# Optimization experiments

Hardware: AMD Instinct MI355X
Metric: run time of the kernel (lower is better)

## Reference

```python
import jax, jax.numpy as jnp
import numpy as np

K = 20
EPS = 1e-5
SLOPE = 0.2

def _knn_idx(x, k):
    # x: [B, C, N] -> idx [B, N, k] of nearest neighbors (includes self)
    xx = jnp.sum(x * x, axis=1)                      # [B, N]
    inner = jnp.einsum('bcn,bcm->bnm', x, x)          # [B, N, N]
    dist = xx[:, :, None] - 2.0 * inner + xx[:, None, :]
    _, idx = jax.lax.top_k(-dist, k)                  # [B, N, k]
    return idx

def _get_attention_feature(x, k):
    # x: [B, C, N] -> [B, N, k, 2C] = cat([x_j - x_i, x_i])
    idx = _knn_idx(x, k)
    xt = jnp.transpose(x, (0, 2, 1))                  # [B, N, C]
    nbr = jax.vmap(lambda pts, ids: pts[ids])(xt, idx)  # [B, N, k, C]
    ctr = xt[:, :, None, :]                           # [B, N, 1, C]
    return jnp.concatenate([nbr - ctr, jnp.broadcast_to(ctr, nbr.shape)], axis=-1)

def _gat(feat, W, a):
    # feat: [B, N, k, 2C]; W: [2C, out_c]; a: [4, H] with H = out_c // 4
    B, N, k, _ = feat.shape
    out_c = W.shape[1]
    H = out_c // 4
    hw = jnp.einsum('bnkf,fd->bnkd', feat, W).reshape(B, N, k, H, 4)
    t = jax.nn.leaky_relu(hw, SLOPE)
    logits = jnp.einsum('bnkhd,dh->bnkh', t, a)
    w = jax.nn.softmax(logits, axis=2)                # softmax over neighbors k
    out = jnp.einsum('bnkh,bnkhd->bnhd', w, hw).reshape(B, N, out_c)
    out = jax.nn.leaky_relu(out, SLOPE)
    return jnp.transpose(out, (0, 2, 1))              # [B, out_c, N]

def _bn(x, gamma, beta):
    # BatchNorm1d in training mode (batch stats) over [B, C, N]
    mu = jnp.mean(x, axis=(0, 2), keepdims=True)
    var = jnp.var(x, axis=(0, 2), keepdims=True)
    xn = (x - mu) / jnp.sqrt(var + EPS)
    return xn * gamma[None, :, None] + beta[None, :, None]

def _layer(x, W, a, gamma, beta):
    feat = _get_attention_feature(x, K)
    h = _gat(feat, W, a)
    h = _bn(h, gamma, beta)
    return jax.nn.leaky_relu(h, SLOPE)

def setup_inputs() -> dict:
    key = jax.random.key(0)
    ks = jax.random.split(key, 10)
    dims = [(3, 64), (64, 64), (64, 128)]
    inp = {'x': jax.random.normal(ks[0], (8, 3, 2048), dtype=jnp.float32)}
    for i, (cin, cout) in enumerate(dims):
        inp[f'W{i}'] = jax.random.normal(ks[1 + 3 * i], (2 * cin, cout), dtype=jnp.float32) * 0.1
        inp[f'a{i}'] = jax.random.normal(ks[2 + 3 * i], (4, cout // 4), dtype=jnp.float32) * 0.1
        inp[f'g{i}'] = jnp.ones((cout,), dtype=jnp.float32)
        inp[f'b{i}'] = jnp.zeros((cout,), dtype=jnp.float32)
    return inp

def reference(x, W0, a0, g0, b0, W1, a1, g1, b1, W2, a2, g2, b2):
    x = _layer(x, W0, a0, g0, b0)
    x = _layer(x, W1, a1, g1, b1)
    x = _layer(x, W2, a2, g2, b2)
    return x  # [B, 128, N]
```

## Files before the change

kernel.cpp:

```cpp
#include <hip/hip_runtime.h>
#include <float.h>
#include <math.h>

#define BATCH 8
#define NPTS  2048
#define KNN   20
#define BN    (BATCH*NPTS)
#define SLOPE 0.2f
#define BNEPS 1e-5f

__global__ void xx_kernel(const float* __restrict__ x, float* __restrict__ xx, int C) {
    int p = blockIdx.x * 256 + threadIdx.x;
    int b = p >> 11, n = p & (NPTS - 1);
    const float* xb = x + (size_t)b * C * NPTS;
    float s = 0.f;
    for (int c = 0; c < C; ++c) { float v = xb[(size_t)c * NPTS + n]; s = fmaf(v, v, s); }
    xx[p] = s;
}

__device__ __forceinline__ void gload_lds16(const float* g, float* l) {
    __builtin_amdgcn_global_load_lds(
        (const __attribute__((address_space(1))) void*)g,
        (__attribute__((address_space(3))) void*)l, 16, 0, 0);
}

template<int C>
__global__ __launch_bounds__(256, 2) void knn8_kernel(const float* __restrict__ x,
                                                      const float* __restrict__ xx,
                                                      float* __restrict__ pv,
                                                      int* __restrict__ pi) {
    constexpr int ROWS = 32, CHUNK = 128, HALF = 1024, NCH = HALF / CHUNK;
    constexpr int CP     = (C > 32) ? 32 : C;
    constexpr int PASSES = C / CP;
    constexpr int NST    = (CP * 32 + 255) / 256;

    __shared__ __align__(16) float xrT[C][32];
    __shared__ __align__(16) union ULX {
        struct { float xc[CP][CHUNK]; float dt[ROWS][129]; float thrG[8][32]; } s;
        struct { float v[8][KNN][ROWS]; unsigned short i[8][KNN][ROWS]; } L;
    } u;

    int t    = threadIdx.x;
    int b    = blockIdx.x >> 7;
    int tile = (blockIdx.x >> 1) & 63;
    int half = blockIdx.x & 1;
    int r0   = tile * ROWS;
    int j0h  = half * HALF;
    const float* xb  = x  + (size_t)b * C * NPTS;
    const float* xxb = xx + (size_t)b * NPTS;

    int ty = t >> 5, tx = t & 31;
    int ty4 = ty * 4, tx4 = tx * 4;

    for (int f = t; f < ROWS * C; f += 256) {
        int r = f & 31, c = f >> 5;
        xrT[c][r] = xb[(size_t)c * NPTS + r0 + r];
    }
    u.s.thrG[ty][tx] = FLT_MAX;
#pragma unroll
    for (int k = 0; k < NST; ++k) {
        int i = t + 256 * k;
        if (i < CP * 32) {
            int c = i >> 5, j = (i & 31) * 4;
            gload_lds16(xb + (size_t)c * NPTS + j0h + j, &u.s.xc[0][0] + (size_t)i * 4);
        }
    }

    float lv[KNN]; int li[KNN];
#pragma unroll
    for (int s = 0; s < KNN; ++s) { lv[s] = FLT_MAX; li[s] = 0x7fffffff; }

    __syncthreads();

    for (int ch = 0; ch < NCH; ++ch) {
        int j0g = j0h + ch * CHUNK;

        float4 a0 = {0,0,0,0}, a1 = {0,0,0,0}, a2 = {0,0,0,0}, a3 = {0,0,0,0};

#pragma unroll 4
        for (int c = 0; c < CP; ++c) {
            float4 rv = *(const float4*)&xrT[c][ty4];
            float4 cv = *(const float4*)&u.s.xc[c][tx4];
            a0.x = fmaf(rv.x, cv.x, a0.x); a0.y = fmaf(rv.x, cv.y, a0.y);
            a0.z = fmaf(rv.x, cv.z, a0.z); a0.w = fmaf(rv.x, cv.w, a0.w);
            a1.x = fmaf(rv.y, cv.x, a1.x); a1.y = fmaf(rv.y, cv.y, a1.y);
            a1.z = fmaf(rv.y, cv.z, a1.z); a1.w = fmaf(rv.y, cv.w, a1.w);
            a2.x = fmaf(rv.z, cv.x, a2.x); a2.y = fmaf(rv.z, cv.y, a2.y);
            a2.z = fmaf(rv.z, cv.z, a2.z); a2.w = fmaf(rv.z, cv.w, a2.w);
            a3.x = fmaf(rv.w, cv.x, a3.x); a3.y = fmaf(rv.w, cv.y, a3.y);
            a3.z = fmaf(rv.w, cv.z, a3.z); a3.w = fmaf(rv.w, cv.w, a3.w);
        }

        if constexpr (PASSES == 2) {
            __syncthreads();
#pragma unroll
            for (int k = 0; k < NST; ++k) {
                int i = t + 256 * k;
                int c = i >> 5, j = (i & 31) * 4;
                gload_lds16(xb + (size_t)(CP + c) * NPTS + j0g + j,
                            &u.s.xc[0][0] + (size_t)i * 4);
            }
            __syncthreads();
#pragma unroll 4
            for (int c = 0; c < CP; ++c) {
                float4 rv = *(const float4*)&xrT[CP + c][ty4];
                float4 cv = *(const float4*)&u.s.xc[c][tx4];
                a0.x = fmaf(rv.x, cv.x, a0.x); a0.y = fmaf(rv.x, cv.y, a0.y);
                a0.z = fmaf(rv.x, cv.z, a0.z); a0.w = fmaf(rv.x, cv.w, a0.w);
                a1.x = fmaf(rv.y, cv.x, a1.x); a1.y = fmaf(rv.y, cv.y, a1.y);
                a1.z = fmaf(rv.y, cv.z, a1.z); a1.w = fmaf(rv.y, cv.w, a1.w);
                a2.x = fmaf(rv.z, cv.x, a2.x); a2.y = fmaf(rv.z, cv.y, a2.y);
                a2.z = fmaf(rv.z, cv.z, a2.z); a2.w = fmaf(rv.z, cv.w, a2.w);
                a3.x = fmaf(rv.w, cv.x, a3.x); a3.y = fmaf(rv.w, cv.y, a3.y);
                a3.z = fmaf(rv.w, cv.z, a3.z); a3.w = fmaf(rv.w, cv.w, a3.w);
            }
        }

        {
            float4 xq = *(const float4*)&xxb[j0g + tx4];
            u.s.dt[ty4 + 0][tx4 + 0] = xq.x - 2.f * a0.x;
            u.s.dt[ty4 + 0][tx4 + 1] = xq.y - 2.f * a0.y;
            u.s.dt[ty4 + 0][tx4 + 2] = xq.z - 2.f * a0.z;
            u.s.dt[ty4 + 0][tx4 + 3] = xq.w - 2.f * a0.w;
            u.s.dt[ty4 + 1][tx4 + 0] = xq.x - 2.f * a1.x;
            u.s.dt[ty4 + 1][tx4 + 1] = xq.y - 2.f * a1.y;
            u.s.dt[ty4 + 1][tx4 + 2] = xq.z - 2.f * a1.z;
            u.s.dt[ty4 + 1][tx4 + 3] = xq.w - 2.f * a1.w;
            u.s.dt[ty4 + 2][tx4 + 0] = xq.x - 2.f * a2.x;
            u.s.dt[ty4 + 2][tx4 + 1] = xq.y - 2.f * a2.y;
            u.s.dt[ty4 + 2][tx4 + 2] = xq.z - 2.f * a2.z;
            u.s.dt[ty4 + 2][tx4 + 3] = xq.w - 2.f * a2.w;
            u.s.dt[ty4 + 3][tx4 + 0] = xq.x - 2.f * a3.x;
            u.s.dt[ty4 + 3][tx4 + 1] = xq.y - 2.f * a3.y;
            u.s.dt[ty4 + 3][tx4 + 2] = xq.z - 2.f * a3.z;
            u.s.dt[ty4 + 3][tx4 + 3] = xq.w - 2.f * a3.w;
        }
        __syncthreads();

        if (ch + 1 < NCH) {
            int j0n = j0g + CHUNK;
#pragma unroll
            for (int k = 0; k < NST; ++k) {
                int i = t + 256 * k;
                if (i < CP * 32) {
                    int c = i >> 5, j = (i & 31) * 4;
                    gload_lds16(xb + (size_t)c * NPTS + j0n + j,
                                &u.s.xc[0][0] + (size_t)i * 4);
                }
            }
        }

        {
            int r = tx;
            float thr = u.s.thrG[0][r];
#pragma unroll
            for (int g = 1; g < 8; ++g) thr = fminf(thr, u.s.thrG[g][r]);

            const float* drow = &u.s.dt[r][ty * 16];
#pragma unroll
            for (int m = 0; m < 16; ++m) {
                float v = drow[m];
                if (v < lv[KNN - 1] && v <= thr) {
                    lv[KNN - 1] = v; li[KNN - 1] = j0g + ty * 16 + m;
#pragma unroll
                    for (int s = KNN - 1; s > 0; --s) {
                        if (lv[s] < lv[s - 1]) {
                            float tv = lv[s]; lv[s] = lv[s - 1]; lv[s - 1] = tv;
                            int   ti = li[s]; li[s] = li[s - 1]; li[s - 1] = ti;
                        }
                    }
                }
            }
        }
        u.s.thrG[ty][tx] = lv[KNN - 1];
        __syncthreads();
    }

    {
        int r = tx, g = ty;
#pragma unroll
        for (int s = 0; s < KNN; ++s) {
            u.L.v[g][s][r] = lv[s];
            u.L.i[g][s][r] = (unsigned short)(li[s] & 0xFFFF);
        }
    }
    __syncthreads();

    if (t < ROWS) {
        int r = t;
        float hv[8]; int hi[8]; int pp[8];
#pragma unroll
        for (int g = 0; g < 8; ++g) { pp[g] = 0; hv[g] = u.L.v[g][0][r]; hi[g] = u.L.i[g][0][r]; }
        size_t base = ((size_t)(b * NPTS + r0 + r) * 2 + half) * KNN;
        for (int o = 0; o < KNN; ++o) {
            float bv = hv[0]; int bi = hi[0]; int bg = 0;
#pragma unroll
            for (int g = 1; g < 8; ++g)
                if (hv[g] < bv || (hv[g] == bv && hi[g] < bi)) { bv = hv[g]; bi = hi[g]; bg = g; }
            pv[base + o] = bv; pi[base + o] = bi;
#pragma unroll
            for (int g = 0; g < 8; ++g)
                if (bg == g) {
                    ++pp[g];
                    bool ok = pp[g] < KNN;
                    int q = ok ? pp[g] : KNN - 1;
                    float nv = u.L.v[g][q][r]; int ni = u.L.i[g][q][r];
                    hv[g] = ok ? nv : FLT_MAX;
                    hi[g] = ok ? ni : 0x7fffffff;
                }
        }
    }
}

__global__ void knnmerge_kernel(const float* __restrict__ pv, const int* __restrict__ pi,
                                int* __restrict__ idx) {
    int p = blockIdx.x * 256 + threadIdx.x;
    size_t b0 = (size_t)p * 2 * KNN, b1 = b0 + KNN;
    int ia = 0, ib = 0;
    int* op = idx + (size_t)p * KNN;
    for (int o = 0; o < KNN; ++o) {
        float va = pv[b0 + ia], vb = pv[b1 + ib];
        int   ja = pi[b0 + ia], jb = pi[b1 + ib];
        bool takeA = (va < vb) || (va == vb && ja < jb);
        op[o] = takeA ? ja : jb;
        ia += takeA ? 1 : 0;
        ib += takeA ? 0 : 1;
    }
}

__global__ void proj_kernel(const float* __restrict__ x, const float* __restrict__ W,
                            float* __restrict__ y, float* __restrict__ z, int C, int Cout) {
    int p = blockIdx.x;
    int b = p >> 11, n = p & (NPTS - 1);
    int j = threadIdx.x;
    __shared__ float xc[64];
    if (j < C) xc[j] = x[(size_t)b * C * NPTS + (size_t)j * NPTS + n];
    __syncthreads();
    float sy = 0.f, sz = 0.f;
    for (int c = 0; c < C; ++c) {
        float xv = xc[c];
        float wt = W[c * Cout + j];
        float wb = W[(C + c) * Cout + j];
        sy = fmaf(xv, wt, sy);
        sz = fmaf(xv, wb - wt, sz);
    }
    y[(size_t)p * Cout + j] = sy;
    z[(size_t)p * Cout + j] = sz;
}

template<int CO>
__global__ __launch_bounds__(256) void attn_kernel(const float* __restrict__ y,
                                                   const float* __restrict__ z,
                                                   const int* __restrict__ idx,
                                                   const float* __restrict__ a,
                                                   float* __restrict__ hout) {
    constexpr int NCH = CO / 64;
    constexpr int H   = CO / 4;
    int wv = threadIdx.x >> 6;
    int l  = threadIdx.x & 63;
    int p  = blockIdx.x * 4 + wv;
    int b  = p >> 11;
    float hw[NCH][KNN], lg[NCH][KNN], zv[NCH], av[NCH];
#pragma unroll
    for (int q = 0; q < NCH; ++q) {
        int c = l + 64 * q;
        zv[q] = z[(size_t)p * CO + c];
        av[q] = a[(c & 3) * H + (c >> 2)];
    }
    const int* ip = idx + (size_t)p * KNN;
#pragma unroll
    for (int j = 0; j < KNN; ++j) {
        int m = ip[j];
        const float* yr = y + ((size_t)(b * NPTS) + m) * CO;
#pragma unroll
        for (int q = 0; q < NCH; ++q) {
            int c = l + 64 * q;
            float v = yr[c] + zv[q];
            hw[q][j] = v;
            float tt = v > 0.f ? v : v * SLOPE;
            float part = tt * av[q];
            part += __shfl_xor(part, 1);
            part += __shfl_xor(part, 2);
            lg[q][j] = part;
        }
    }
#pragma unroll
    for (int q = 0; q < NCH; ++q) {
        float mx = -FLT_MAX;
#pragma unroll
        for (int j = 0; j < KNN; ++j) mx = fmaxf(mx, lg[q][j]);
        float s = 0.f;
#pragma unroll
        for (int j = 0; j < KNN; ++j) { float e = expf(lg[q][j] - mx); lg[q][j] = e; s += e; }
        float inv = 1.f / s;
        float o = 0.f;
#pragma unroll
        for (int j = 0; j < KNN; ++j) o = fmaf(lg[q][j] * inv, hw[q][j], o);
        o = o > 0.f ? o : o * SLOPE;
        int c = l + 64 * q;
        hout[(size_t)p * CO + c] = o;
    }
}

__global__ void bnstatA_kernel(const float* __restrict__ h, float* __restrict__ part, int CO) {
    __shared__ float s1[256], s2[256];
    int g = blockIdx.x, t = threadIdx.x;
    int c = t & (CO - 1), sub = t / CO;
    int nsub = 256 / CO;
    const int ppb = BN / 64;
    float a1 = 0.f, a2 = 0.f;
    for (int i = 0; i < ppb / nsub; ++i) {
        int p = g * ppb + sub + i * nsub;
        float v = h[(size_t)p * CO + c];
        a1 += v; a2 = fmaf(v, v, a2);
    }
    s1[t] = a1; s2[t] = a2;
    __syncthreads();
    if (sub == 0) {
        for (int k = 1; k < nsub; ++k) { a1 += s1[k * CO + c]; a2 += s2[k * CO + c]; }
        part[(size_t)g * CO + c]        = a1;
        part[(size_t)(64 + g) * CO + c] = a2;
    }
}

__global__ void bnstatB_kernel(const float* __restrict__ part, float* __restrict__ mu,
                               float* __restrict__ rstd, int CO) {
    int c = threadIdx.x;
    float s1 = 0.f, s2 = 0.f;
    for (int g = 0; g < 64; ++g) { s1 += part[(size_t)g * CO + c]; s2 += part[(size_t)(64 + g) * CO + c]; }
    float m   = s1 / (float)BN;
    float var = s2 / (float)BN - m * m;
    mu[c]   = m;
    rstd[c] = 1.f / sqrtf(var + BNEPS);
}

template<int CO>
__global__ __launch_bounds__(256) void bnapply_kernel(const float* __restrict__ h,
                                                      const float* __restrict__ mu,
                                                      const float* __restrict__ rstd,
                                                      const float* __restrict__ gamma,
                                                      const float* __restrict__ beta,
                                                      float* __restrict__ xout) {
    __shared__ float tile[64][CO + 1];
    int g  = blockIdx.x;
    int p0 = g * 64;
    int b  = p0 >> 11, n0 = p0 & (NPTS - 1);
    int t  = threadIdx.x;
    for (int fi = t; fi < 64 * CO; fi += 256) {
        int pt = fi / CO, c = fi % CO;
        tile[pt][c] = h[(size_t)(p0 + pt) * CO + c];
    }
    __syncthreads();
    for (int fi = t; fi < 64 * CO; fi += 256) {
        int c = fi >> 6, nn = fi & 63;
        float v = tile[nn][c];
        v = (v - mu[c]) * rstd[c] * gamma[c] + beta[c];
        v = v > 0.f ? v : v * SLOPE;
        xout[((size_t)b * CO + c) * NPTS + n0 + nn] = v;
    }
}

static void run_layer(const float* xin, const float* W, const float* a,
                      const float* gm, const float* bt, float* xout, int C, int CO,
                      float* xx, float* pv, int* pi, int* idx, float* y, float* z, float* h,
                      float* part, float* mu, float* rstd, hipStream_t stream) {
    xx_kernel<<<BN / 256, 256, 0, stream>>>(xin, xx, C);
    if (C == 3)
        knn8_kernel<3><<<BATCH * 128, 256, 0, stream>>>(xin, xx, pv, pi);
    else
        knn8_kernel<64><<<BATCH * 128, 256, 0, stream>>>(xin, xx, pv, pi);
    knnmerge_kernel<<<BN / 256, 256, 0, stream>>>(pv, pi, idx);
    proj_kernel<<<BN, CO, 0, stream>>>(xin, W, y, z, C, CO);
    if (CO == 64)
        attn_kernel<64><<<BN / 4, 256, 0, stream>>>(y, z, idx, a, h);
    else
        attn_kernel<128><<<BN / 4, 256, 0, stream>>>(y, z, idx, a, h);
    bnstatA_kernel<<<64, 256, 0, stream>>>(h, part, CO);
    bnstatB_kernel<<<1, CO, 0, stream>>>(part, mu, rstd, CO);
    if (CO == 64)
        bnapply_kernel<64><<<BN / 64, 256, 0, stream>>>(h, mu, rstd, gm, bt, xout);
    else
        bnapply_kernel<128><<<BN / 64, 256, 0, stream>>>(h, mu, rstd, gm, bt, xout);
}

extern "C" void kernel_launch(void* const* d_in, const int* in_sizes, int n_in,
                              void* d_out, int out_size, void* d_ws, size_t ws_size,
                              hipStream_t stream) {
    const float* x  = (const float*)d_in[0];
    const float* W[3]  = {(const float*)d_in[1], (const float*)d_in[5], (const float*)d_in[9]};
    const float* a[3]  = {(const float*)d_in[2], (const float*)d_in[6], (const float*)d_in[10]};
    const float* gm[3] = {(const float*)d_in[3], (const float*)d_in[7], (const float*)d_in[11]};
    const float* bt[3] = {(const float*)d_in[4], (const float*)d_in[8], (const float*)d_in[12]};

    char* base = (char*)d_ws;
    size_t off = 0;
    auto carve = [&](size_t bytes) -> void* {
        void* r = base + off;
        off = (off + bytes + 255) & ~(size_t)255;
        return r;
    };
    float* xx   = (float*)carve((size_t)BN * sizeof(float));
    float* pv   = (float*)carve((size_t)BN * 2 * KNN * sizeof(float));
    int*   pi   = (int*)  carve((size_t)BN * 2 * KNN * sizeof(int));
    int*   idx  = (int*)  carve((size_t)BN * KNN * sizeof(int));
    float* y    = (float*)carve((size_t)BN * 128 * sizeof(float));
    float* z    = (float*)carve((size_t)BN * 128 * sizeof(float));
    float* h    = (float*)carve((size_t)BN * 128 * sizeof(float));
    float* part = (float*)carve((size_t)128 * 128 * sizeof(float));
    float* mu   = (float*)carve(128 * sizeof(float));
    float* rstd = (float*)carve(128 * sizeof(float));
    float* x1   = (float*)carve((size_t)BATCH * 64 * NPTS * sizeof(float));
    float* x2   = (float*)carve((size_t)BATCH * 64 * NPTS * sizeof(float));
    float* out  = (float*)d_out;

    run_layer(x,  W[0], a[0], gm[0], bt[0], x1,  3,  64, xx, pv, pi, idx, y, z, h, part, mu, rstd, stream);
    run_layer(x1, W[1], a[1], gm[1], bt[1], x2,  64, 64, xx, pv, pi, idx, y, z, h, part, mu, rstd, stream);
    run_layer(x2, W[2], a[2], gm[2], bt[2], out, 64, 128, xx, pv, pi, idx, y, z, h, part, mu, rstd, stream);
}
```

Baseline: 780.9 us.

## Shrink KNN distance chunk to 64 columns and drop the two-pass channel split

Halves the candidate chunk to 64 columns so all channels fit in shared memory at once, removing the two-pass channel loop and its extra barriers for C=64. Each thread now computes a 4x2 register tile and writes it as float2 stores, and xrT is padded to 33 to reduce bank conflicts. In exchange the loop runs twice as many chunks with twice as many barriers and prefetches, and per-FMA reuse of the row values is lower.

```diff
diff --git a/kernel.cpp b/kernel.cpp
--- a/kernel.cpp
+++ b/kernel.cpp
@@ -25,18 +25,16 @@
 }
 
 template<int C>
-__global__ __launch_bounds__(256, 2) void knn8_kernel(const float* __restrict__ x,
-                                                      const float* __restrict__ xx,
-                                                      float* __restrict__ pv,
-                                                      int* __restrict__ pi) {
-    constexpr int ROWS = 32, CHUNK = 128, HALF = 1024, NCH = HALF / CHUNK;
-    constexpr int CP     = (C > 32) ? 32 : C;
-    constexpr int PASSES = C / CP;
-    constexpr int NST    = (CP * 32 + 255) / 256;
-
-    __shared__ __align__(16) float xrT[C][32];
+__global__ __launch_bounds__(256, 2) void knn11_kernel(const float* __restrict__ x,
+                                                       const float* __restrict__ xx,
+                                                       float* __restrict__ pv,
+                                                       int* __restrict__ pi) {
+    constexpr int ROWS = 32, CHUNK = 64, HALF = 1024, NCH = HALF / CHUNK;
+    constexpr int NST  = (C * 16 + 255) / 256;
+
+    __shared__ __align__(16) float xrT[C][33];
     __shared__ __align__(16) union ULX {
-        struct { float xc[CP][CHUNK]; float dt[ROWS][129]; float thrG[8][32]; } s;
+        struct { float xc[C][CHUNK]; float dt[ROWS][65]; float thrG[8][32]; } s;
         struct { float v[8][KNN][ROWS]; unsigned short i[8][KNN][ROWS]; } L;
     } u;
 
@@ -50,7 +48,7 @@
     const float* xxb = xx + (size_t)b * NPTS;
 
     int ty = t >> 5, tx = t & 31;
-    int ty4 = ty * 4, tx4 = tx * 4;
+    int ty4 = ty * 4, tx2 = tx * 2;
 
     for (int f = t; f < ROWS * C; f += 256) {
         int r = f & 31, c = f >> 5;
@@ -60,8 +58,8 @@
 #pragma unroll
     for (int k = 0; k < NST; ++k) {
         int i = t + 256 * k;
-        if (i < CP * 32) {
-            int c = i >> 5, j = (i & 31) * 4;
+        if (i < C * 16) {
+            int c = i >> 4, j = (i & 15) * 4;
             gload_lds16(xb + (size_t)c * NPTS + j0h + j, &u.s.xc[0][0] + (size_t)i * 4);
         }
     }
@@ -73,77 +71,39 @@
     __syncthreads();
 
     for (int ch = 0; ch < NCH; ++ch) {
-        int j0g = j0h + ch * CHUNK;
-
-        float4 a0 = {0,0,0,0}, a1 = {0,0,0,0}, a2 = {0,0,0,0}, a3 = {0,0,0,0};
-
+        int j0 = j0h + ch * CHUNK;
+
+        float2 a0 = {0,0}, a1 = {0,0}, a2 = {0,0}, a3 = {0,0};
 #pragma unroll 4
-        for (int c = 0; c < CP; ++c) {
+        for (int c = 0; c < C; ++c) {
             float4 rv = *(const float4*)&xrT[c][ty4];
-            float4 cv = *(const float4*)&u.s.xc[c][tx4];
+            float2 cv = *(const float2*)&u.s.xc[c][tx2];
             a0.x = fmaf(rv.x, cv.x, a0.x); a0.y = fmaf(rv.x, cv.y, a0.y);
-            a0.z = fmaf(rv.x, cv.z, a0.z); a0.w = fmaf(rv.x, cv.w, a0.w);
             a1.x = fmaf(rv.y, cv.x, a1.x); a1.y = fmaf(rv.y, cv.y, a1.y);
-            a1.z = fmaf(rv.y, cv.z, a1.z); a1.w = fmaf(rv.y, cv.w, a1.w);
             a2.x = fmaf(rv.z, cv.x, a2.x); a2.y = fmaf(rv.z, cv.y, a2.y);
-            a2.z = fmaf(rv.z, cv.z, a2.z); a2.w = fmaf(rv.z, cv.w, a2.w);
             a3.x = fmaf(rv.w, cv.x, a3.x); a3.y = fmaf(rv.w, cv.y, a3.y);
-            a3.z = fmaf(rv.w, cv.z, a3.z); a3.w = fmaf(rv.w, cv.w, a3.w);
-        }
-
-        if constexpr (PASSES == 2) {
-            __syncthreads();
+        }
+        {
+            float2 xq = *(const float2*)&xxb[j0 + tx2];
+            float2 w;
+            w.x = xq.x - 2.f * a0.x; w.y = xq.y - 2.f * a0.y;
+            *(float2*)&u.s.dt[ty4 + 0][tx2] = w;
+            w.x = xq.x - 2.f * a1.x; w.y = xq.y - 2.f * a1.y;
+            *(float2*)&u.s.dt[ty4 + 1][tx2] = w;
+            w.x = xq.x - 2.f * a2.x; w.y = xq.y - 2.f * a2.y;
+            *(float2*)&u.s.dt[ty4 + 2][tx2] = w;
+            w.x = xq.x - 2.f * a3.x; w.y = xq.y - 2.f * a3.y;
+            *(float2*)&u.s.dt[ty4 + 3][tx2] = w;
+        }
+        __syncthreads();
+
+        if (ch + 1 < NCH) {
+            int j0n = j0 + CHUNK;
 #pragma unroll
             for (int k = 0; k < NST; ++k) {
                 int i = t + 256 * k;
-                int c = i >> 5, j = (i & 31) * 4;
-                gload_lds16(xb + (size_t)(CP + c) * NPTS + j0g + j,
-                            &u.s.xc[0][0] + (size_t)i * 4);
-            }
-            __syncthreads();
-#pragma unroll 4
-            for (int c = 0; c < CP; ++c) {
-                float4 rv = *(const float4*)&xrT[CP + c][ty4];
-                float4 cv = *(const float4*)&u.s.xc[c][tx4];
-                a0.x = fmaf(rv.x, cv.x, a0.x); a0.y = fmaf(rv.x, cv.y, a0.y);
-                a0.z = fmaf(rv.x, cv.z, a0.z); a0.w = fmaf(rv.x, cv.w, a0.w);
-                a1.x = fmaf(rv.y, cv.x, a1.x); a1.y = fmaf(rv.y, cv.y, a1.y);
-                a1.z = fmaf(rv.y, cv.z, a1.z); a1.w = fmaf(rv.y, cv.w, a1.w);
-                a2.x = fmaf(rv.z, cv.x, a2.x); a2.y = fmaf(rv.z, cv.y, a2.y);
-                a2.z = fmaf(rv.z, cv.z, a2.z); a2.w = fmaf(rv.z, cv.w, a2.w);
-                a3.x = fmaf(rv.w, cv.x, a3.x); a3.y = fmaf(rv.w, cv.y, a3.y);
-                a3.z = fmaf(rv.w, cv.z, a3.z); a3.w = fmaf(rv.w, cv.w, a3.w);
-            }
-        }
-
-        {
-            float4 xq = *(const float4*)&xxb[j0g + tx4];
-            u.s.dt[ty4 + 0][tx4 + 0] = xq.x - 2.f * a0.x;
-            u.s.dt[ty4 + 0][tx4 + 1] = xq.y - 2.f * a0.y;
-            u.s.dt[ty4 + 0][tx4 + 2] = xq.z - 2.f * a0.z;
-            u.s.dt[ty4 + 0][tx4 + 3] = xq.w - 2.f * a0.w;
-            u.s.dt[ty4 + 1][tx4 + 0] = xq.x - 2.f * a1.x;
-            u.s.dt[ty4 + 1][tx4 + 1] = xq.y - 2.f * a1.y;
-            u.s.dt[ty4 + 1][tx4 + 2] = xq.z - 2.f * a1.z;
-            u.s.dt[ty4 + 1][tx4 + 3] = xq.w - 2.f * a1.w;
-            u.s.dt[ty4 + 2][tx4 + 0] = xq.x - 2.f * a2.x;
-            u.s.dt[ty4 + 2][tx4 + 1] = xq.y - 2.f * a2.y;
-            u.s.dt[ty4 + 2][tx4 + 2] = xq.z - 2.f * a2.z;
-            u.s.dt[ty4 + 2][tx4 + 3] = xq.w - 2.f * a2.w;
-            u.s.dt[ty4 + 3][tx4 + 0] = xq.x - 2.f * a3.x;
-            u.s.dt[ty4 + 3][tx4 + 1] = xq.y - 2.f * a3.y;
-            u.s.dt[ty4 + 3][tx4 + 2] = xq.z - 2.f * a3.z;
-            u.s.dt[ty4 + 3][tx4 + 3] = xq.w - 2.f * a3.w;
-        }
-        __syncthreads();
-
-        if (ch + 1 < NCH) {
-            int j0n = j0g + CHUNK;
-#pragma unroll
-            for (int k = 0; k < NST; ++k) {
-                int i = t + 256 * k;
-                if (i < CP * 32) {
-                    int c = i >> 5, j = (i & 31) * 4;
+                if (i < C * 16) {
+                    int c = i >> 4, j = (i & 15) * 4;
                     gload_lds16(xb + (size_t)c * NPTS + j0n + j,
                                 &u.s.xc[0][0] + (size_t)i * 4);
                 }
@@ -156,12 +116,12 @@
 #pragma unroll
             for (int g = 1; g < 8; ++g) thr = fminf(thr, u.s.thrG[g][r]);
 
-            const float* drow = &u.s.dt[r][ty * 16];
-#pragma unroll
-            for (int m = 0; m < 16; ++m) {
+            const float* drow = &u.s.dt[r][ty * 8];
+#pragma unroll
+            for (int m = 0; m < 8; ++m) {
                 float v = drow[m];
                 if (v < lv[KNN - 1] && v <= thr) {
-                    lv[KNN - 1] = v; li[KNN - 1] = j0g + ty * 16 + m;
+                    lv[KNN - 1] = v; li[KNN - 1] = j0 + ty * 8 + m;
 #pragma unroll
                     for (int s = KNN - 1; s > 0; --s) {
                         if (lv[s] < lv[s - 1]) {
@@ -366,9 +326,9 @@
                       float* part, float* mu, float* rstd, hipStream_t stream) {
     xx_kernel<<<BN / 256, 256, 0, stream>>>(xin, xx, C);
     if (C == 3)
-        knn8_kernel<3><<<BATCH * 128, 256, 0, stream>>>(xin, xx, pv, pi);
+        knn11_kernel<3><<<BATCH * 128, 256, 0, stream>>>(xin, xx, pv, pi);
     else
-        knn8_kernel<64><<<BATCH * 128, 256, 0, stream>>>(xin, xx, pv, pi);
+        knn11_kernel<64><<<BATCH * 128, 256, 0, stream>>>(xin, xx, pv, pi);
     knnmerge_kernel<<<BN / 256, 256, 0, stream>>>(pv, pi, idx);
     proj_kernel<<<BN, CO, 0, stream>>>(xin, W, y, z, C, CO);
     if (CO == 64)
```

Result: slower. 803.5 us (+2.9%).
